# Performance work log

Measured on AMD Instinct MI355X. Metric: run time of the kernel, lower is better.

## Reference

```python
import jax, jax.numpy as jnp
import numpy as np

D_IN = 1024
D_OUT = 1024
NUM_HEADS = 16
HEAD_DIM = D_OUT // NUM_HEADS
SEQ = 2048
BATCH = 4


def setup_inputs() -> dict:
    key = jax.random.key(0)
    ks = jax.random.split(key, 6)
    s_in = 1.0 / np.sqrt(D_IN)
    s_out = 1.0 / np.sqrt(D_OUT)
    return {
        "inputs": jax.random.normal(ks[0], (BATCH, SEQ, D_IN), dtype=jnp.float32),
        # nn.Linear stores weight as [out, in]; y = x @ W.T
        "W_q": jax.random.uniform(ks[1], (D_OUT, D_IN), jnp.float32, -s_in, s_in),
        "W_k": jax.random.uniform(ks[2], (D_OUT, D_IN), jnp.float32, -s_in, s_in),
        "W_v": jax.random.uniform(ks[3], (D_OUT, D_IN), jnp.float32, -s_in, s_in),
        "W_o": jax.random.uniform(ks[4], (D_OUT, D_OUT), jnp.float32, -s_out, s_out),
        "b_o": jax.random.uniform(ks[5], (D_OUT,), jnp.float32, -s_out, s_out),
    }


def reference(inputs, W_q, W_k, W_v, W_o, b_o):
    B, T, _ = inputs.shape
    # projections: [B, T, d_out] -> [B, H, T, hd]
    def split_heads(x):
        return x.reshape(B, T, NUM_HEADS, HEAD_DIM).transpose(0, 2, 1, 3)

    Q = split_heads(inputs @ W_q.T)
    K = split_heads(inputs @ W_k.T)
    V = split_heads(inputs @ W_v.T)

    # [B, H, T, T] causal attention scores
    scores = jnp.einsum("bhqd,bhkd->bhqk", Q, K)
    causal = jnp.tril(jnp.ones((T, T), dtype=bool))  # True = keep
    scores = jnp.where(causal, scores, -jnp.inf)
    weights = jax.nn.softmax(scores / np.sqrt(HEAD_DIM), axis=-1)
    # dropout p=0.0 (eval mode): identity

    ctx = jnp.einsum("bhqk,bhkd->bhqd", weights, V)
    ctx = ctx.transpose(0, 2, 1, 3).reshape(B, T, D_OUT)
    return ctx @ W_o.T + b_o
```

## Files before the change

### kernel.cpp

```cpp
#include <hip/hip_runtime.h>
#include <cstdint>
#include <cstddef>

#define D_MODEL 1024
#define SEQQ    2048
#define NBATCH  4
#define NHEAD   16
#define HDIM    64
#define MTOT    (NBATCH * SEQQ)

typedef __attribute__((ext_vector_type(8))) short short8;
typedef __attribute__((ext_vector_type(4))) float floatx4;
typedef unsigned short u16;

__device__ __forceinline__ u16 f2bf(float f) {
  union { float f; uint32_t u; } a; a.f = f;
  uint32_t u = a.u;
  u += 0x7fffu + ((u >> 16) & 1u);
  return (u16)(u >> 16);
}

__device__ __forceinline__ floatx4 mfma16(short8 a, short8 b, floatx4 c) {
  return __builtin_amdgcn_mfma_f32_16x16x32_bf16(a, b, c, 0, 0, 0);
}

__device__ __forceinline__ void load_lds16(const void* g, void* l) {
  __builtin_amdgcn_global_load_lds(
      (const __attribute__((address_space(1))) uint32_t*)g,
      (__attribute__((address_space(3))) uint32_t*)l, 16, 0, 0);
}

__global__ __launch_bounds__(256) void k_cast_all(
    const float* __restrict__ X, const float* __restrict__ w0,
    const float* __restrict__ w1, const float* __restrict__ w2,
    const float* __restrict__ w3,
    u16* __restrict__ xb, u16* __restrict__ y0, u16* __restrict__ y1,
    u16* __restrict__ y2, u16* __restrict__ y3) {
  const int bx = blockIdx.x;
  const float* src; u16* dst; int i;
  if (bx < 8192) {
    src = X; dst = xb; i = (bx * 256 + threadIdx.x) * 4;
  } else {
    const int w = (bx - 8192) >> 10;
    src = (w == 0) ? w0 : (w == 1) ? w1 : (w == 2) ? w2 : w3;
    dst = (w == 0) ? y0 : (w == 1) ? y1 : (w == 2) ? y2 : y3;
    i = (((bx - 8192) & 1023) * 256 + threadIdx.x) * 4;
  }
  float4 v = *(const float4*)(src + i);
  ushort4 o;
  o.x = f2bf(v.x); o.y = f2bf(v.y); o.z = f2bf(v.z); o.w = f2bf(v.w);
  *(ushort4*)(dst + i) = o;
}

__global__ __launch_bounds__(256) void k_gemm_bt(
    const u16* __restrict__ A,
    const u16* __restrict__ B0, const u16* __restrict__ B1, const u16* __restrict__ B2,
    void* __restrict__ C0, void* __restrict__ C1, u16* __restrict__ VtOut,
    const float* __restrict__ bias, int M, int N, int K, int f32out, float ascaleQ) {
  __shared__ __align__(16) u16 As[128 * 64];
  __shared__ __align__(16) u16 Bs[128 * 64];
  const int tid = threadIdx.x;
  const int lane = tid & 63, wave = tid >> 6;
  const int quad = lane >> 4, l15 = lane & 15;
  const int m0 = blockIdx.y * 128, n0 = blockIdx.x * 128;
  const int wr = wave >> 1, wc = wave & 1;
  const u16* Bm = (blockIdx.z == 0) ? B0 : (blockIdx.z == 1 ? B1 : B2);
  void* Cm = (blockIdx.z == 0) ? C0 : C1;
  const float ascale = (blockIdx.z == 0) ? ascaleQ : 1.0f;

  floatx4 acc[4][4];
#pragma unroll
  for (int i = 0; i < 4; ++i)
#pragma unroll
    for (int j = 0; j < 4; ++j) acc[i][j] = (floatx4){0.f, 0.f, 0.f, 0.f};

  const int srow = tid >> 3;
  const int scolx = ((tid & 7) * 8) ^ ((srow & 7) * 8);
  const u16* Ag = A + (size_t)(m0 + srow) * K + scolx;
  const u16* Bg = Bm + (size_t)(n0 + srow) * K + scolx;

  for (int kt = 0; kt < K; kt += 64) {
    __syncthreads();
#pragma unroll
    for (int p = 0; p < 4; ++p) {
      load_lds16(Ag + (size_t)(p * 32) * K + kt, &As[p * 2048 + wave * 512]);
      load_lds16(Bg + (size_t)(p * 32) * K + kt, &Bs[p * 2048 + wave * 512]);
    }
    __syncthreads();

    short8 af[2][4], bfg[2][4];
#pragma unroll
    for (int ks = 0; ks < 2; ++ks) {
      const int kkx = (ks * 32 + quad * 8) ^ ((l15 & 7) * 8);
#pragma unroll
      for (int i = 0; i < 4; ++i) {
        af[ks][i]  = *(const short8*)&As[(wr * 64 + i * 16 + l15) * 64 + kkx];
        bfg[ks][i] = *(const short8*)&Bs[(wc * 64 + i * 16 + l15) * 64 + kkx];
      }
    }
#pragma unroll
    for (int ks = 0; ks < 2; ++ks)
#pragma unroll
      for (int mi = 0; mi < 4; ++mi)
#pragma unroll
        for (int ni = 0; ni < 4; ++ni)
          acc[mi][ni] = mfma16(af[ks][mi], bfg[ks][ni], acc[mi][ni]);
  }

  if (blockIdx.z == 2) {
#pragma unroll
    for (int mi = 0; mi < 4; ++mi) {
#pragma unroll
      for (int ni = 0; ni < 4; ++ni) {
        const int row = m0 + wr * 64 + mi * 16 + quad * 4;
        const int col = n0 + wc * 64 + ni * 16 + l15;
        const int b = row >> 11, t = row & 2047;
        const int h = col >> 6, d = col & 63;
        ushort4 pk;
        pk.x = f2bf(acc[mi][ni][0]); pk.y = f2bf(acc[mi][ni][1]);
        pk.z = f2bf(acc[mi][ni][2]); pk.w = f2bf(acc[mi][ni][3]);
        *(ushort4*)(VtOut + (((size_t)(b * 16 + h) * 64 + d) * SEQQ + t)) = pk;
      }
    }
    return;
  }
#pragma unroll
  for (int mi = 0; mi < 4; ++mi) {
#pragma unroll
    for (int ni = 0; ni < 4; ++ni) {
      const int row = m0 + wr * 64 + mi * 16 + quad * 4;
      const int col = n0 + wc * 64 + ni * 16 + l15;
      const float bv = bias ? bias[col] : 0.f;
#pragma unroll
      for (int r = 0; r < 4; ++r) {
        const float v = acc[mi][ni][r] * ascale + bv;
        if (f32out) ((float*)Cm)[(size_t)(row + r) * N + col] = v;
        else        ((u16*)Cm)[(size_t)(row + r) * N + col] = f2bf(v);
      }
    }
  }
}

__device__ __forceinline__ short8 mk8(uint32_t a, uint32_t b, uint32_t c, uint32_t d) {
  union { uint32_t u[4]; short8 s; } t;
  t.u[0] = a; t.u[1] = b; t.u[2] = c; t.u[3] = d;
  return t.s;
}

__device__ __forceinline__ void softmax_reg(
    const floatx4 (&st)[4], float& lp, uint32_t (&w)[4][2]) {
#pragma unroll
  for (int ni = 0; ni < 4; ++ni) {
    const float p0 = __builtin_amdgcn_exp2f(st[ni][0]);
    const float p1 = __builtin_amdgcn_exp2f(st[ni][1]);
    const float p2 = __builtin_amdgcn_exp2f(st[ni][2]);
    const float p3 = __builtin_amdgcn_exp2f(st[ni][3]);
    lp += (p0 + p1) + (p2 + p3);
    w[ni][0] = __builtin_amdgcn_perm(__float_as_uint(p1), __float_as_uint(p0), 0x07060302u);
    w[ni][1] = __builtin_amdgcn_perm(__float_as_uint(p3), __float_as_uint(p2), 0x07060302u);
  }
}

__device__ __forceinline__ short8 pf_prep(const uint32_t (&w)[4][2], int kc) {
  uint32_t y0 = w[2 * kc][0], z0 = w[2 * kc + 1][0];
  asm("v_permlane32_swap_b32 %0, %1" : "+v"(y0), "+v"(z0));
  asm("v_permlane16_swap_b32 %0, %1" : "+v"(y0), "+v"(z0));
  uint32_t y1 = w[2 * kc][1], z1 = w[2 * kc + 1][1];
  asm("v_permlane32_swap_b32 %0, %1" : "+v"(y1), "+v"(z1));
  asm("v_permlane16_swap_b32 %0, %1" : "+v"(y1), "+v"(z1));
  return mk8(y0, y1, z0, z1);
}

__global__ __launch_bounds__(512) void k_attn(
    const u16* __restrict__ Q, const u16* __restrict__ Kg,
    const u16* __restrict__ Vt, u16* __restrict__ O) {
  __shared__ __align__(16) u16 Ks[2][64 * 64];
  __shared__ __align__(16) u16 Vs[2][64 * 64];
  const int tid = threadIdx.x, lane = tid & 63, wave = tid >> 6;
  const int quad = lane >> 4, l15 = lane & 15;

  const int lin = blockIdx.x;
  const int c = lin & 255, k2 = lin >> 8;
  const int g = k2 ? (7 - (c & 7)) : (c & 7);
  const int bh = (c >> 3) | (k2 << 5);
  const int b = bh >> 4, h = bh & 15;

  const int wgrp = wave >> 2, wsub = wave & 3;
  const int a = 2 * g + wgrp;
  const int qwA = 64 * a + wsub * 16;
  const int qwB = SEQQ - 64 * (a + 1) + wsub * 16;
  const int nT = 32 - 2 * g;
  const int lastB = 31 - a;

  const u16* kbase = Kg + (size_t)(b * SEQQ) * D_MODEL + h * HDIM;
  const u16* vbase = Vt + (size_t)bh * (HDIM * SEQQ);

  const int srow = tid >> 3;
  const int scol = ((tid & 7) * 8) ^ ((srow & 7) * 8);

  {
    load_lds16(kbase + (size_t)srow * D_MODEL + scol, &Ks[0][wave * 512]);
    load_lds16(vbase + (size_t)srow * SEQQ + scol,    &Vs[0][wave * 512]);
  }

  short8 qfA[2], qfB[2];
  {
    const u16* qa = Q + (size_t)(b * SEQQ + qwA + l15) * D_MODEL + h * HDIM;
    const u16* qb = Q + (size_t)(b * SEQQ + qwB + l15) * D_MODEL + h * HDIM;
#pragma unroll
    for (int ks = 0; ks < 2; ++ks) {
      qfA[ks] = *(const short8*)(qa + ks * 32 + quad * 8);
      qfB[ks] = *(const short8*)(qb + ks * 32 + quad * 8);
    }
  }

  floatx4 accA[4], accB[4];
  float lAp = 0.f, lBp = 0.f;
#pragma unroll
  for (int i = 0; i < 4; ++i) {
    accA[i] = (floatx4){0.f, 0.f, 0.f, 0.f};
    accB[i] = (floatx4){0.f, 0.f, 0.f, 0.f};
  }

  for (int t = 0; t < nT; ++t) {
    const int cur = t & 1;
    __syncthreads();
    if (t + 1 < nT) {
      const int kt1 = (t + 1) * 64, nxt = cur ^ 1;
      load_lds16(kbase + (size_t)(kt1 + srow) * D_MODEL + scol, &Ks[nxt][wave * 512]);
      load_lds16(vbase + (size_t)srow * SEQQ + kt1 + scol,      &Vs[nxt][wave * 512]);
    }
    const int kt = t * 64;

    short8 kf[4][2];
#pragma unroll
    for (int ni = 0; ni < 4; ++ni)
#pragma unroll
      for (int ks = 0; ks < 2; ++ks)
        kf[ni][ks] = *(const short8*)&Ks[cur][(ni * 16 + l15) * 64 +
                                            ((ks * 32 + quad * 8) ^ ((l15 & 7) * 8))];
    short8 vf[2][4];
#pragma unroll
    for (int kc = 0; kc < 2; ++kc)
#pragma unroll
      for (int di = 0; di < 4; ++di)
        vf[kc][di] = *(const short8*)&Vs[cur][(di * 16 + l15) * 64 +
                                             ((kc * 32 + quad * 8) ^ ((l15 & 7) * 8))];

    const bool doA = (t <= a);
    const bool doB = (t <= lastB);
    uint32_t wA[4][2], wB[4][2];
    if (doA) {
      floatx4 st[4];
#pragma unroll
      for (int ni = 0; ni < 4; ++ni) {
        floatx4 s = (floatx4){0.f, 0.f, 0.f, 0.f};
        s = mfma16(kf[ni][0], qfA[0], s);
        s = mfma16(kf[ni][1], qfA[1], s);
        st[ni] = s;
      }
      if (t == a) {
        const int qg = qwA + l15;
#pragma unroll
        for (int ni = 0; ni < 4; ++ni) {
          const int kg = kt + ni * 16 + quad * 4;
#pragma unroll
          for (int r = 0; r < 4; ++r)
            if (kg + r > qg) st[ni][r] = -1e30f;
        }
      }
      softmax_reg(st, lAp, wA);
    }
    if (doB) {
      floatx4 st[4];
#pragma unroll
      for (int ni = 0; ni < 4; ++ni) {
        floatx4 s = (floatx4){0.f, 0.f, 0.f, 0.f};
        s = mfma16(kf[ni][0], qfB[0], s);
        s = mfma16(kf[ni][1], qfB[1], s);
        st[ni] = s;
      }
      if (t == lastB) {
        const int qg = qwB + l15;
#pragma unroll
        for (int ni = 0; ni < 4; ++ni) {
          const int kg = kt + ni * 16 + quad * 4;
#pragma unroll
          for (int r = 0; r < 4; ++r)
            if (kg + r > qg) st[ni][r] = -1e30f;
        }
      }
      softmax_reg(st, lBp, wB);
    }
#pragma unroll
    for (int kc = 0; kc < 2; ++kc) {
      if (doA) {
        const short8 pfA = pf_prep(wA, kc);
#pragma unroll
        for (int di = 0; di < 4; ++di)
          accA[di] = mfma16(pfA, vf[kc][di], accA[di]);
      }
      if (doB) {
        const short8 pfB = pf_prep(wB, kc);
#pragma unroll
        for (int di = 0; di < 4; ++di)
          accB[di] = mfma16(pfB, vf[kc][di], accB[di]);
      }
    }
  }

  lAp += __shfl_xor(lAp, 16); lAp += __shfl_xor(lAp, 32);
  lBp += __shfl_xor(lBp, 16); lBp += __shfl_xor(lBp, 32);

  {
    u16* orow = O + (size_t)(b * SEQQ + qwA + quad * 4) * D_MODEL + h * HDIM + l15;
#pragma unroll
    for (int r = 0; r < 4; ++r) {
      const float inv = 1.0f / __shfl(lAp, quad * 4 + r, 16);
#pragma unroll
      for (int di = 0; di < 4; ++di)
        orow[(size_t)r * D_MODEL + di * 16] = f2bf(accA[di][r] * inv);
    }
  }
  {
    u16* orow = O + (size_t)(b * SEQQ + qwB + quad * 4) * D_MODEL + h * HDIM + l15;
#pragma unroll
    for (int r = 0; r < 4; ++r) {
      const float inv = 1.0f / __shfl(lBp, quad * 4 + r, 16);
#pragma unroll
      for (int di = 0; di < 4; ++di)
        orow[(size_t)r * D_MODEL + di * 16] = f2bf(accB[di][r] * inv);
    }
  }
}

extern "C" void kernel_launch(void* const* d_in, const int* in_sizes, int n_in,
                              void* d_out, int out_size, void* d_ws, size_t ws_size,
                              hipStream_t stream) {
  const float* X  = (const float*)d_in[0];
  const float* Wq = (const float*)d_in[1];
  const float* Wk = (const float*)d_in[2];
  const float* Wv = (const float*)d_in[3];
  const float* Wo = (const float*)d_in[4];
  const float* bo = (const float*)d_in[5];
  float* out = (float*)d_out;

  u16* ws = (u16*)d_ws;
  const size_t NE = (size_t)MTOT * D_MODEL;
  u16* Xb  = ws;
  u16* Qb  = Xb + NE;
  u16* Kb  = Qb + NE;
  u16* Vt  = Kb + NE;
  u16* Cb  = Vt + NE;
  u16* Wqb = Cb + NE;
  u16* Wkb = Wqb + (size_t)D_MODEL * D_MODEL;
  u16* Wvb = Wkb + (size_t)D_MODEL * D_MODEL;
  u16* Wob = Wvb + (size_t)D_MODEL * D_MODEL;

  const float SCL2E = 0.18033688f;

  k_cast_all<<<12288, 256, 0, stream>>>(X, Wq, Wk, Wv, Wo, Xb, Wqb, Wkb, Wvb, Wob);

  k_gemm_bt<<<dim3(D_MODEL / 128, MTOT / 128, 3), 256, 0, stream>>>(
      Xb, Wqb, Wkb, Wvb, Qb, Kb, Vt, nullptr, MTOT, D_MODEL, D_MODEL, 0, SCL2E);

  k_attn<<<512, 512, 0, stream>>>(Qb, Kb, Vt, Cb);

  k_gemm_bt<<<dim3(D_MODEL / 128, MTOT / 128, 1), 256, 0, stream>>>(
      Cb, Wob, Wob, Wob, out, out, nullptr, bo, MTOT, D_MODEL, D_MODEL, 1, 1.0f);
}
```

Measured before the change: 274.6 us.

## Stage 128-key K/V tiles per barrier and raise wave priority around MFMAs

The attention loop now loads 128 keys of K and V into double-buffered LDS per iteration, then runs two 64-key sub-steps. This halves the number of __syncthreads barriers and global-to-LDS staging rounds. It also wraps the MFMA sequences in s_setprio so matrix work is favoured over other waves' instructions. LDS use doubles to 64KB per block, which can lower occupancy.

```diff
diff --git a/kernel.cpp b/kernel.cpp
--- a/kernel.cpp
+++ b/kernel.cpp
@@ -174,8 +174,8 @@
 __global__ __launch_bounds__(512) void k_attn(
     const u16* __restrict__ Q, const u16* __restrict__ Kg,
     const u16* __restrict__ Vt, u16* __restrict__ O) {
-  __shared__ __align__(16) u16 Ks[2][64 * 64];
-  __shared__ __align__(16) u16 Vs[2][64 * 64];
+  __shared__ __align__(16) u16 Ks[2][128 * 64];
+  __shared__ __align__(16) u16 Vs[2][64 * 128];
   const int tid = threadIdx.x, lane = tid & 63, wave = tid >> 6;
   const int quad = lane >> 4, l15 = lane & 15;
 
@@ -189,19 +189,32 @@
   const int a = 2 * g + wgrp;
   const int qwA = 64 * a + wsub * 16;
   const int qwB = SEQQ - 64 * (a + 1) + wsub * 16;
-  const int nT = 32 - 2 * g;
-  const int lastB = 31 - a;
+  const int nT = 16 - g;
+  const int uB = 31 - a;
 
   const u16* kbase = Kg + (size_t)(b * SEQQ) * D_MODEL + h * HDIM;
   const u16* vbase = Vt + (size_t)bh * (HDIM * SEQQ);
 
-  const int srow = tid >> 3;
-  const int scol = ((tid & 7) * 8) ^ ((srow & 7) * 8);
-
-  {
-    load_lds16(kbase + (size_t)srow * D_MODEL + scol, &Ks[0][wave * 512]);
-    load_lds16(vbase + (size_t)srow * SEQQ + scol,    &Vs[0][wave * 512]);
-  }
+  const int krow = tid >> 3;
+  const int kcol = ((tid & 7) * 8) ^ ((krow & 7) * 8);
+  const int vrow = tid >> 4;
+  const int vslot = tid & 15;
+  const int vcol = (vslot >> 3) * 64 + (((vslot & 7) ^ (vrow & 7)) * 8);
+
+#define STAGE_KV(tt, buf)                                                           \
+  {                                                                                 \
+    const int kt_ = (tt) * 128;                                                     \
+    load_lds16(kbase + (size_t)(kt_ + krow) * D_MODEL + kcol,                       \
+               &Ks[buf][wave * 512]);                                               \
+    load_lds16(kbase + (size_t)(kt_ + 64 + krow) * D_MODEL + kcol,                  \
+               &Ks[buf][4096 + wave * 512]);                                        \
+    load_lds16(vbase + (size_t)vrow * SEQQ + kt_ + vcol,                            \
+               &Vs[buf][wave * 512]);                                               \
+    load_lds16(vbase + (size_t)(32 + vrow) * SEQQ + kt_ + vcol,                     \
+               &Vs[buf][4096 + wave * 512]);                                        \
+  }
+
+  STAGE_KV(0, 0);
 
   short8 qfA[2], qfB[2];
   {
@@ -225,86 +238,94 @@
   for (int t = 0; t < nT; ++t) {
     const int cur = t & 1;
     __syncthreads();
-    if (t + 1 < nT) {
-      const int kt1 = (t + 1) * 64, nxt = cur ^ 1;
-      load_lds16(kbase + (size_t)(kt1 + srow) * D_MODEL + scol, &Ks[nxt][wave * 512]);
-      load_lds16(vbase + (size_t)srow * SEQQ + kt1 + scol,      &Vs[nxt][wave * 512]);
-    }
-    const int kt = t * 64;
-
-    short8 kf[4][2];
-#pragma unroll
-    for (int ni = 0; ni < 4; ++ni)
-#pragma unroll
-      for (int ks = 0; ks < 2; ++ks)
-        kf[ni][ks] = *(const short8*)&Ks[cur][(ni * 16 + l15) * 64 +
-                                            ((ks * 32 + quad * 8) ^ ((l15 & 7) * 8))];
-    short8 vf[2][4];
-#pragma unroll
-    for (int kc = 0; kc < 2; ++kc)
-#pragma unroll
-      for (int di = 0; di < 4; ++di)
-        vf[kc][di] = *(const short8*)&Vs[cur][(di * 16 + l15) * 64 +
-                                             ((kc * 32 + quad * 8) ^ ((l15 & 7) * 8))];
-
-    const bool doA = (t <= a);
-    const bool doB = (t <= lastB);
-    uint32_t wA[4][2], wB[4][2];
-    if (doA) {
-      floatx4 st[4];
-#pragma unroll
-      for (int ni = 0; ni < 4; ++ni) {
-        floatx4 s = (floatx4){0.f, 0.f, 0.f, 0.f};
-        s = mfma16(kf[ni][0], qfA[0], s);
-        s = mfma16(kf[ni][1], qfA[1], s);
-        st[ni] = s;
-      }
-      if (t == a) {
-        const int qg = qwA + l15;
+    if (t + 1 < nT) STAGE_KV(t + 1, cur ^ 1);
+
+#pragma unroll
+    for (int sub = 0; sub < 2; ++sub) {
+      const int u = 2 * t + sub;
+      const bool doA = (u <= a);
+      const bool doB = (u <= uB);
+
+      short8 kf[4][2];
+#pragma unroll
+      for (int ni = 0; ni < 4; ++ni)
+#pragma unroll
+        for (int ks = 0; ks < 2; ++ks)
+          kf[ni][ks] = *(const short8*)&Ks[cur][(sub * 64 + ni * 16 + l15) * 64 +
+                                               ((ks * 32 + quad * 8) ^ ((l15 & 7) * 8))];
+      short8 vf[2][4];
+#pragma unroll
+      for (int kc = 0; kc < 2; ++kc)
+#pragma unroll
+        for (int di = 0; di < 4; ++di)
+          vf[kc][di] = *(const short8*)&Vs[cur][(di * 16 + l15) * 128 + sub * 64 +
+                                               ((kc * 32 + quad * 8) ^ ((l15 & 7) * 8))];
+
+      uint32_t wA[4][2], wB[4][2];
+      if (doA) {
+        floatx4 st[4];
+        __builtin_amdgcn_s_setprio(1);
 #pragma unroll
         for (int ni = 0; ni < 4; ++ni) {
-          const int kg = kt + ni * 16 + quad * 4;
-#pragma unroll
-          for (int r = 0; r < 4; ++r)
-            if (kg + r > qg) st[ni][r] = -1e30f;
-        }
-      }
-      softmax_reg(st, lAp, wA);
-    }
-    if (doB) {
-      floatx4 st[4];
-#pragma unroll
-      for (int ni = 0; ni < 4; ++ni) {
-        floatx4 s = (floatx4){0.f, 0.f, 0.f, 0.f};
-        s = mfma16(kf[ni][0], qfB[0], s);
-        s = mfma16(kf[ni][1], qfB[1], s);
-        st[ni] = s;
-      }
-      if (t == lastB) {
-        const int qg = qwB + l15;
+          floatx4 s = (floatx4){0.f, 0.f, 0.f, 0.f};
+          s = mfma16(kf[ni][0], qfA[0], s);
+          s = mfma16(kf[ni][1], qfA[1], s);
+          st[ni] = s;
+        }
+        __builtin_amdgcn_s_setprio(0);
+        if (u == a) {
+          const int qg = qwA + l15;
+#pragma unroll
+          for (int ni = 0; ni < 4; ++ni) {
+            const int kg = u * 64 + ni * 16 + quad * 4;
+#pragma unroll
+            for (int r = 0; r < 4; ++r)
+              if (kg + r > qg) st[ni][r] = -1e30f;
+          }
+        }
+        softmax_reg(st, lAp, wA);
+      }
+      if (doB) {
+        floatx4 st[4];
+        __builtin_amdgcn_s_setprio(1);
 #pragma unroll
         for (int ni = 0; ni < 4; ++ni) {
-          const int kg = kt + ni * 16 + quad * 4;
-#pragma unroll
-          for (int r = 0; r < 4; ++r)
-            if (kg + r > qg) st[ni][r] = -1e30f;
-        }
-      }
-      softmax_reg(st, lBp, wB);
-    }
-#pragma unroll
-    for (int kc = 0; kc < 2; ++kc) {
-      if (doA) {
-        const short8 pfA = pf_prep(wA, kc);
-#pragma unroll
-        for (int di = 0; di < 4; ++di)
-          accA[di] = mfma16(pfA, vf[kc][di], accA[di]);
-      }
-      if (doB) {
-        const short8 pfB = pf_prep(wB, kc);
-#pragma unroll
-        for (int di = 0; di < 4; ++di)
-          accB[di] = mfma16(pfB, vf[kc][di], accB[di]);
+          floatx4 s = (floatx4){0.f, 0.f, 0.f, 0.f};
+          s = mfma16(kf[ni][0], qfB[0], s);
+          s = mfma16(kf[ni][1], qfB[1], s);
+          st[ni] = s;
+        }
+        __builtin_amdgcn_s_setprio(0);
+        if (u == uB) {
+          const int qg = qwB + l15;
+#pragma unroll
+          for (int ni = 0; ni < 4; ++ni) {
+            const int kg = u * 64 + ni * 16 + quad * 4;
+#pragma unroll
+            for (int r = 0; r < 4; ++r)
+              if (kg + r > qg) st[ni][r] = -1e30f;
+          }
+        }
+        softmax_reg(st, lBp, wB);
+      }
+#pragma unroll
+      for (int kc = 0; kc < 2; ++kc) {
+        if (doA) {
+          const short8 pfA = pf_prep(wA, kc);
+          __builtin_amdgcn_s_setprio(1);
+#pragma unroll
+          for (int di = 0; di < 4; ++di)
+            accA[di] = mfma16(pfA, vf[kc][di], accA[di]);
+          __builtin_amdgcn_s_setprio(0);
+        }
+        if (doB) {
+          const short8 pfB = pf_prep(wB, kc);
+          __builtin_amdgcn_s_setprio(1);
+#pragma unroll
+          for (int di = 0; di < 4; ++di)
+            accB[di] = mfma16(pfB, vf[kc][di], accB[di]);
+          __builtin_amdgcn_s_setprio(0);
+        }
       }
     }
   }
```

New measurement: 271.4 us. No clear change (-1.2%).
